# Kernel tuning notes

Measured on AMD Instinct MI355X. Metric: run time of the kernel, lower is better.

Reference implementation:

```python
import jax, jax.numpy as jnp
import numpy as np
import math

B, L, Dk, Dv, Hs, Ws = 8, 8, 256, 128, 48, 64  # Hs=H//8, Ws=W//8
ALPHA = 1.0
TRAIN_SZ = 1000
# scale = log_{train_sz}(L*Hs*Ws + Hs*Ws) / sqrt(Dk)
SCALE = math.log(L * Hs * Ws + Hs * Ws) / math.log(TRAIN_SZ) / math.sqrt(Dk)


def setup_inputs() -> dict:
    key = jax.random.key(0)
    ks = jax.random.split(key, 7)
    xav = lambda k, d: jax.random.uniform(k, (d, d), jnp.float32, -1.0, 1.0) * math.sqrt(6.0 / (2 * d))
    return {
        "fc": jax.random.normal(ks[0], (B, Dk, Hs, Ws), jnp.float32),
        "fm": jax.random.normal(ks[1], (B, Dv, Hs, Ws), jnp.float32),
        "key_buffer": jax.random.normal(ks[2], (B, L, Dk, Hs, Ws), jnp.float32),
        "value_buffer": jax.random.normal(ks[3], (B, L, Dv, Hs, Ws), jnp.float32),
        "Q": xav(ks[4], Dk),
        "K": xav(ks[5], Dk),
        "V": xav(ks[6], Dv),
    }


def reference(fc, fm, key_buffer, value_buffer, Q, K, V):
    # matmul over channel dim: 'ijkl,jm->imkl'
    mm = lambda a, W: jnp.einsum('bdhw,de->behw', a, W)
    q = mm(fc, Q)  # [B, Dk, Hs, Ws]
    # FIFO buffer shift (buffers and new frames are detached in the original)
    new_k = jax.lax.stop_gradient(mm(fc, K))  # [B, Dk, Hs, Ws]
    new_v = jax.lax.stop_gradient(mm(fm, V))  # [B, Dv, Hs, Ws]
    kb = jnp.concatenate([jax.lax.stop_gradient(key_buffer)[:, 1:], new_k[:, None]], axis=1)   # [B, L, Dk, Hs, Ws]
    vb = jnp.concatenate([jax.lax.stop_gradient(value_buffer)[:, 1:], new_v[:, None]], axis=1)  # [B, L, Dv, Hs, Ws]
    # per-pixel scores over memory dim: 'ijkl,imjkl->imkl'
    scores = SCALE * jnp.einsum('bdhw,bldhw->blhw', q, kb)  # [B, L, Hs, Ws]
    # NOTE: original applies softmax over dim=-1, i.e. the WIDTH axis (faithful)
    attn = jax.nn.softmax(scores, axis=-1)
    # combine over memory dim: 'imkl,imnkl->inkl'
    out = jnp.einsum('blhw,blehw->behw', attn, vb)  # [B, Dv, Hs, Ws]
    return fm + ALPHA * out
```

## Files before the change

### kernel.cpp

```cpp
#include <hip/hip_runtime.h>
#include <math.h>

#define B_ 8
#define L_ 8
#define DK 256
#define DV 128
#define HS 48
#define WS_ 64
#define HW 3072
#define QSTRIDE 786432
#define VSTRIDE 393216

#define KS 16
#define BE 64
#define BP 128

#define FMA4(acc, s, v) { acc.x += (s)*(v).x; acc.y += (s)*(v).y; acc.z += (s)*(v).z; acc.w += (s)*(v).w; }

__global__ __launch_bounds__(256) void gemm_tn(const float* __restrict__ W,
                                               const float* __restrict__ X,
                                               float* __restrict__ C,
                                               int D, int E) {
    const int P = HW;
    const int bp = blockIdx.x * BP;
    const int be = blockIdx.y * BE;
    const int b  = blockIdx.z;
    X += (size_t)b * D * P;
    C += (size_t)b * E * P;

    __shared__ float Ws[KS][BE];
    __shared__ float Xs[KS][BP];

    const int tid = threadIdx.x;
    const int tx = tid & 15;
    const int ty = tid >> 4;

    float4 acc0[4] = {};
    float4 acc1[4] = {};

    for (int d0 = 0; d0 < D; d0 += KS) {
        __syncthreads();
        {
            int row = tid >> 4, col = tid & 15;
            *(float4*)&Ws[row][col * 4] =
                *(const float4*)&W[(size_t)(d0 + row) * E + be + col * 4];
        }
        {
            int f = tid;
            int row = f >> 5, col = f & 31;
            *(float4*)&Xs[row][col * 4] =
                *(const float4*)&X[(size_t)(d0 + row) * P + bp + col * 4];
            f = tid + 256; row = f >> 5; col = f & 31;
            *(float4*)&Xs[row][col * 4] =
                *(const float4*)&X[(size_t)(d0 + row) * P + bp + col * 4];
        }
        __syncthreads();
        #pragma unroll
        for (int k = 0; k < KS; ++k) {
            float4 a  = *(float4*)&Ws[k][ty * 4];
            float4 b0 = *(float4*)&Xs[k][tx * 8];
            float4 b1 = *(float4*)&Xs[k][tx * 8 + 4];
            FMA4(acc0[0], a.x, b0); FMA4(acc1[0], a.x, b1);
            FMA4(acc0[1], a.y, b0); FMA4(acc1[1], a.y, b1);
            FMA4(acc0[2], a.z, b0); FMA4(acc1[2], a.z, b1);
            FMA4(acc0[3], a.w, b0); FMA4(acc1[3], a.w, b1);
        }
    }
    #pragma unroll
    for (int i = 0; i < 4; ++i) {
        int e = be + ty * 4 + i;
        *(float4*)&C[(size_t)e * P + bp + tx * 8]     = acc0[i];
        *(float4*)&C[(size_t)e * P + bp + tx * 8 + 4] = acc1[i];
    }
}

__global__ __launch_bounds__(64) void scores_kernel(const float* __restrict__ q,
                                                    const float* __restrict__ knew,
                                                    const float* __restrict__ key_buffer,
                                                    float* __restrict__ attn,
                                                    float scale) {
    const int bx = blockIdx.x;
    const int b = bx / (L_ * HS);
    const int rem = bx % (L_ * HS);
    const int l = rem / HS;
    const int h = rem % HS;

    const int lane = threadIdx.x;
    const int p4 = lane & 15;
    const int dq = lane >> 4;

    const float* qbase = q + (size_t)b * QSTRIDE + h * WS_;
    const float* kbase = (l < 7)
        ? key_buffer + (size_t)(b * L_ + l + 1) * QSTRIDE + h * WS_
        : knew + (size_t)b * QSTRIDE + h * WS_;

    const float* kp = kbase + (size_t)(dq * 64) * HW + p4 * 4;
    const float* qp = qbase + (size_t)(dq * 64) * HW + p4 * 4;

    float4 s = {0.f, 0.f, 0.f, 0.f};
    #pragma unroll 8
    for (int d = 0; d < 64; ++d) {
        float4 kv = *(const float4*)kp; kp += HW;
        float4 qv = *(const float4*)qp; qp += HW;
        s.x += qv.x * kv.x; s.y += qv.y * kv.y;
        s.z += qv.z * kv.z; s.w += qv.w * kv.w;
    }
    #pragma unroll
    for (int off = 16; off <= 32; off <<= 1) {
        s.x += __shfl_xor(s.x, off);
        s.y += __shfl_xor(s.y, off);
        s.z += __shfl_xor(s.z, off);
        s.w += __shfl_xor(s.w, off);
    }
    s.x *= scale; s.y *= scale; s.z *= scale; s.w *= scale;

    float m = fmaxf(fmaxf(s.x, s.y), fmaxf(s.z, s.w));
    #pragma unroll
    for (int off = 1; off <= 8; off <<= 1) m = fmaxf(m, __shfl_xor(m, off));
    float4 e;
    e.x = __expf(s.x - m); e.y = __expf(s.y - m);
    e.z = __expf(s.z - m); e.w = __expf(s.w - m);
    float sum = e.x + e.y + e.z + e.w;
    #pragma unroll
    for (int off = 1; off <= 8; off <<= 1) sum += __shfl_xor(sum, off);
    float inv = 1.0f / sum;
    e.x *= inv; e.y *= inv; e.z *= inv; e.w *= inv;

    if (dq == 0) {
        *(float4*)&attn[(size_t)((b * L_ + l) * HS + h) * WS_ + p4 * 4] = e;
    }
}

__global__ __launch_bounds__(256) void pv_kernel(const float* __restrict__ attn,
                                                 const float* __restrict__ value_buffer,
                                                 const float* __restrict__ vnew,
                                                 const float* __restrict__ fm,
                                                 float* __restrict__ out) {
    const int bx = blockIdx.x;
    const int b = bx / 96;
    const int rem = bx % 96;
    const int h = rem >> 1;
    const int eh = rem & 1;

    const int tid = threadIdx.x;
    const int p4 = tid & 15;
    const int eg = tid >> 4;
    const int e0 = eh * 64 + eg * 4;

    float4 ar[8];
    #pragma unroll
    for (int l = 0; l < 8; ++l)
        ar[l] = *(const float4*)&attn[(size_t)((b * L_ + l) * HS + h) * WS_ + p4 * 4];

    const float* vb[8];
    #pragma unroll
    for (int l = 0; l < 7; ++l)
        vb[l] = value_buffer + (size_t)(b * L_ + l + 1) * VSTRIDE + h * WS_;
    vb[7] = vnew + (size_t)b * VSTRIDE + h * WS_;

    const float* fmb = fm + (size_t)b * VSTRIDE + h * WS_;
    float* outb = out + (size_t)b * VSTRIDE + h * WS_;

    #pragma unroll
    for (int i = 0; i < 4; ++i) {
        const int e = e0 + i;
        const size_t off = (size_t)e * HW + p4 * 4;
        float4 acc = {0.f, 0.f, 0.f, 0.f};
        #pragma unroll
        for (int l = 0; l < 8; ++l) {
            float4 v = *(const float4*)(vb[l] + off);
            acc.x += ar[l].x * v.x; acc.y += ar[l].y * v.y;
            acc.z += ar[l].z * v.z; acc.w += ar[l].w * v.w;
        }
        float4 f = *(const float4*)(fmb + off);
        f.x += acc.x; f.y += acc.y; f.z += acc.z; f.w += acc.w;
        *(float4*)(outb + off) = f;
    }
}

extern "C" void kernel_launch(void* const* d_in, const int* in_sizes, int n_in,
                              void* d_out, int out_size, void* d_ws, size_t ws_size,
                              hipStream_t stream) {
    const float* fc           = (const float*)d_in[0];
    const float* fm           = (const float*)d_in[1];
    const float* key_buffer   = (const float*)d_in[2];
    const float* value_buffer = (const float*)d_in[3];
    const float* Q            = (const float*)d_in[4];
    const float* K            = (const float*)d_in[5];
    const float* V            = (const float*)d_in[6];
    float* out = (float*)d_out;

    float* ws   = (float*)d_ws;
    float* q    = ws;
    float* knew = ws + 6291456;
    float* vnew = ws + 12582912;
    float* attn = ws + 15728640;

    const float scale = (float)(log(27648.0) / log(1000.0) / 16.0);

    gemm_tn<<<dim3(HW / BP, DK / BE, B_), 256, 0, stream>>>(Q, fc, q, DK, DK);
    gemm_tn<<<dim3(HW / BP, DK / BE, B_), 256, 0, stream>>>(K, fc, knew, DK, DK);
    gemm_tn<<<dim3(HW / BP, DV / BE, B_), 256, 0, stream>>>(V, fm, vnew, DV, DV);

    scores_kernel<<<B_ * L_ * HS, 64, 0, stream>>>(q, knew, key_buffer, attn, scale);

    pv_kernel<<<B_ * HS * 2, 256, 0, stream>>>(attn, value_buffer, vnew, fm, out);
}
```

Measured before the change: 475.8 us.

## Replace FP32 projection GEMMs with split-bf16 MFMA and fuse Q/K projections

Moves the three channel projections from scalar FP32 FMA tiles to MFMA bf16 instructions. The fp32 accuracy is emulated with hi/lo bf16 splitting, using three MFMAs per tile (hi*hi, lo*hi, hi*lo). A prep kernel splits and transposes the weights each call. The Q and K projections are fused into one kernel so fc is read and converted only once. The activation conversion happens in shared memory with a small padded tile, which adds conversion ALU work and narrower transposed LDS stores.

```diff
diff --git a/kernel.cpp b/kernel.cpp
--- a/kernel.cpp
+++ b/kernel.cpp
@@ -1,4 +1,5 @@
 #include <hip/hip_runtime.h>
+#include <hip/hip_bf16.h>
 #include <math.h>
 
 #define B_ 8
@@ -11,66 +12,108 @@
 #define QSTRIDE 786432
 #define VSTRIDE 393216
 
-#define KS 16
-#define BE 64
-#define BP 128
-
-#define FMA4(acc, s, v) { acc.x += (s)*(v).x; acc.y += (s)*(v).y; acc.z += (s)*(v).z; acc.w += (s)*(v).w; }
-
-__global__ __launch_bounds__(256) void gemm_tn(const float* __restrict__ W,
-                                               const float* __restrict__ X,
-                                               float* __restrict__ C,
-                                               int D, int E) {
-    const int P = HW;
-    const int bp = blockIdx.x * BP;
-    const int be = blockIdx.y * BE;
+typedef unsigned short ushort_t;
+typedef __attribute__((ext_vector_type(8))) short short8v;
+typedef __attribute__((ext_vector_type(4))) float float4v;
+
+__global__ __launch_bounds__(256) void prep_weights(
+    const float* __restrict__ Q, const float* __restrict__ K, const float* __restrict__ V,
+    ushort_t* __restrict__ WQh, ushort_t* __restrict__ WQl,
+    ushort_t* __restrict__ WKh, ushort_t* __restrict__ WKl,
+    ushort_t* __restrict__ WVh, ushort_t* __restrict__ WVl) {
+    const int bid = blockIdx.x;
+    const float* W; ushort_t *Wh, *Wl; int D, e;
+    if (bid < 256)      { W = Q; Wh = WQh; Wl = WQl; D = 256; e = bid; }
+    else if (bid < 512) { W = K; Wh = WKh; Wl = WKl; D = 256; e = bid - 256; }
+    else                { W = V; Wh = WVh; Wl = WVl; D = 128; e = bid - 512; }
+    const int d = threadIdx.x;
+    if (d < D) {
+        float x = W[(size_t)d * D + e];
+        __hip_bfloat16 h = __float2bfloat16(x);
+        float hf = __bfloat162float(h);
+        __hip_bfloat16 lo = __float2bfloat16(x - hf);
+        Wh[(size_t)e * D + d] = *(ushort_t*)&h;
+        Wl[(size_t)e * D + d] = *(ushort_t*)&lo;
+    }
+}
+
+template<int NW, int D>
+__global__ __launch_bounds__(256) void gemm_mfma(
+    const float* __restrict__ X,
+    const ushort_t* __restrict__ W1h, const ushort_t* __restrict__ W1l,
+    const ushort_t* __restrict__ W2h, const ushort_t* __restrict__ W2l,
+    float* __restrict__ C1, float* __restrict__ C2) {
+    const int bp = blockIdx.x * 64;
+    const int be = blockIdx.y * 64;
     const int b  = blockIdx.z;
-    X += (size_t)b * D * P;
-    C += (size_t)b * E * P;
-
-    __shared__ float Ws[KS][BE];
-    __shared__ float Xs[KS][BP];
-
-    const int tid = threadIdx.x;
-    const int tx = tid & 15;
-    const int ty = tid >> 4;
-
-    float4 acc0[4] = {};
-    float4 acc1[4] = {};
-
-    for (int d0 = 0; d0 < D; d0 += KS) {
+    X  += (size_t)b * D * HW;
+
+    __shared__ ushort_t Xh[64][40];
+    __shared__ ushort_t Xl[64][40];
+
+    const int tid  = threadIdx.x;
+    const int lane = tid & 63;
+    const int w    = tid >> 6;
+    const int l15  = lane & 15;
+    const int kg   = (lane >> 4) * 8;
+
+    float4v acc1[4] = {};
+    float4v acc2[4] = {};
+
+    const int estrip = be + w * 16;
+    const size_t arow = (size_t)(estrip + l15) * D;
+
+    for (int k0 = 0; k0 < D; k0 += 32) {
         __syncthreads();
-        {
-            int row = tid >> 4, col = tid & 15;
-            *(float4*)&Ws[row][col * 4] =
-                *(const float4*)&W[(size_t)(d0 + row) * E + be + col * 4];
-        }
-        {
-            int f = tid;
-            int row = f >> 5, col = f & 31;
-            *(float4*)&Xs[row][col * 4] =
-                *(const float4*)&X[(size_t)(d0 + row) * P + bp + col * 4];
-            f = tid + 256; row = f >> 5; col = f & 31;
-            *(float4*)&Xs[row][col * 4] =
-                *(const float4*)&X[(size_t)(d0 + row) * P + bp + col * 4];
+        #pragma unroll
+        for (int r = 0; r < 2; ++r) {
+            int v  = tid + 256 * r;
+            int kk = v >> 4;
+            int p4 = (v & 15) * 4;
+            float4 g = *(const float4*)&X[(size_t)(k0 + kk) * HW + bp + p4];
+            float xs[4] = {g.x, g.y, g.z, g.w};
+            #pragma unroll
+            for (int i = 0; i < 4; ++i) {
+                __hip_bfloat16 h = __float2bfloat16(xs[i]);
+                float hf = __bfloat162float(h);
+                __hip_bfloat16 lo = __float2bfloat16(xs[i] - hf);
+                Xh[p4 + i][kk] = *(ushort_t*)&h;
+                Xl[p4 + i][kk] = *(ushort_t*)&lo;
+            }
         }
         __syncthreads();
-        #pragma unroll
-        for (int k = 0; k < KS; ++k) {
-            float4 a  = *(float4*)&Ws[k][ty * 4];
-            float4 b0 = *(float4*)&Xs[k][tx * 8];
-            float4 b1 = *(float4*)&Xs[k][tx * 8 + 4];
-            FMA4(acc0[0], a.x, b0); FMA4(acc1[0], a.x, b1);
-            FMA4(acc0[1], a.y, b0); FMA4(acc1[1], a.y, b1);
-            FMA4(acc0[2], a.z, b0); FMA4(acc1[2], a.z, b1);
-            FMA4(acc0[3], a.w, b0); FMA4(acc1[3], a.w, b1);
-        }
-    }
-    #pragma unroll
-    for (int i = 0; i < 4; ++i) {
-        int e = be + ty * 4 + i;
-        *(float4*)&C[(size_t)e * P + bp + tx * 8]     = acc0[i];
-        *(float4*)&C[(size_t)e * P + bp + tx * 8 + 4] = acc1[i];
+
+        const short8v a1h = *(const short8v*)&W1h[arow + k0 + kg];
+        const short8v a1l = *(const short8v*)&W1l[arow + k0 + kg];
+        short8v a2h, a2l;
+        if (NW == 2) {
+            a2h = *(const short8v*)&W2h[arow + k0 + kg];
+            a2l = *(const short8v*)&W2l[arow + k0 + kg];
+        }
+        #pragma unroll
+        for (int pf = 0; pf < 4; ++pf) {
+            const short8v bh = *(const short8v*)&Xh[pf * 16 + l15][kg];
+            const short8v bl = *(const short8v*)&Xl[pf * 16 + l15][kg];
+            acc1[pf] = __builtin_amdgcn_mfma_f32_16x16x32_bf16(a1h, bh, acc1[pf], 0, 0, 0);
+            acc1[pf] = __builtin_amdgcn_mfma_f32_16x16x32_bf16(a1l, bh, acc1[pf], 0, 0, 0);
+            acc1[pf] = __builtin_amdgcn_mfma_f32_16x16x32_bf16(a1h, bl, acc1[pf], 0, 0, 0);
+            if (NW == 2) {
+                acc2[pf] = __builtin_amdgcn_mfma_f32_16x16x32_bf16(a2h, bh, acc2[pf], 0, 0, 0);
+                acc2[pf] = __builtin_amdgcn_mfma_f32_16x16x32_bf16(a2l, bh, acc2[pf], 0, 0, 0);
+                acc2[pf] = __builtin_amdgcn_mfma_f32_16x16x32_bf16(a2h, bl, acc2[pf], 0, 0, 0);
+            }
+        }
+    }
+
+    #pragma unroll
+    for (int pf = 0; pf < 4; ++pf) {
+        #pragma unroll
+        for (int i = 0; i < 4; ++i) {
+            const int e = estrip + (lane >> 4) * 4 + i;
+            const int p = bp + pf * 16 + l15;
+            C1[((size_t)b * D + e) * HW + p] = acc1[pf][i];
+            if (NW == 2) C2[((size_t)b * D + e) * HW + p] = acc2[pf][i];
+        }
     }
 }
 
@@ -195,14 +238,23 @@
     float* knew = ws + 6291456;
     float* vnew = ws + 12582912;
     float* attn = ws + 15728640;
+    ushort_t* wb = (ushort_t*)(ws + 15925248);
+    ushort_t* WQh = wb;
+    ushort_t* WQl = wb + 65536;
+    ushort_t* WKh = wb + 131072;
+    ushort_t* WKl = wb + 196608;
+    ushort_t* WVh = wb + 262144;
+    ushort_t* WVl = wb + 278528;
 
     const float scale = (float)(log(27648.0) / log(1000.0) / 16.0);
 
-    gemm_tn<<<dim3(HW / BP, DK / BE, B_), 256, 0, stream>>>(Q, fc, q, DK, DK);
-    gemm_tn<<<dim3(HW / BP, DK / BE, B_), 256, 0, stream>>>(K, fc, knew, DK, DK);
-    gemm_tn<<<dim3(HW / BP, DV / BE, B_), 256, 0, stream>>>(V, fm, vnew, DV, DV);
+    prep_weights<<<640, 256, 0, stream>>>(Q, K, V, WQh, WQl, WKh, WKl, WVh, WVl);
+
+    gemm_mfma<2, 256><<<dim3(HW / 64, 4, B_), 256, 0, stream>>>(
+        fc, WQh, WQl, WKh, WKl, q, knew);
+    gemm_mfma<1, 128><<<dim3(HW / 64, 2, B_), 256, 0, stream>>>(
+        fm, WVh, WVl, nullptr, nullptr, vnew, nullptr);
 
     scores_kernel<<<B_ * L_ * HS, 64, 0, stream>>>(q, knew, key_buffer, attn, scale);
-
     pv_kernel<<<B_ * HS * 2, 256, 0, stream>>>(attn, value_buffer, vnew, fm, out);
 }
```

Result: faster. 426.8 us (-10.3%).
